# Kernel optimization log

Hardware: AMD Instinct MI355X
Metric: run time of the kernel (lower is better)

Reference implementation:

```python
import jax, jax.numpy as jnp
import numpy as np
from jax import lax

CIN = 3
NUM_BINS = 9
EPS_MAG = 1e-6
EPS_IN = 1e-5  # torch InstanceNorm2d default eps


def setup_inputs() -> dict:
    key = jax.random.key(0)
    kx, = jax.random.split(key, 1)
    x = jax.random.normal(kx, (32, CIN, 512, 512), dtype=jnp.float32)
    # Sobel kernels, repeated across input channels exactly as in _init_weights
    sx = jnp.array([[-1.0, 0.0, 1.0], [-2.0, 0.0, 2.0], [-1.0, 0.0, 1.0]], jnp.float32)
    sy = jnp.array([[-1.0, -2.0, -1.0], [0.0, 0.0, 0.0], [1.0, 2.0, 1.0]], jnp.float32)
    sobel_x = jnp.broadcast_to(sx, (1, CIN, 3, 3)).astype(jnp.float32)  # OIHW
    sobel_y = jnp.broadcast_to(sy, (1, CIN, 3, 3)).astype(jnp.float32)
    # Orientation 1x1 conv weights: [num_bins, 2] = [cos(theta), sin(theta)]
    angles = jnp.linspace(0.0, np.pi, NUM_BINS + 1)[:-1]
    orient_w = jnp.stack([jnp.cos(angles), jnp.sin(angles)], axis=1).astype(jnp.float32)
    # InstanceNorm affine params (torch init: weight=1, bias=0)
    gamma = jnp.ones((NUM_BINS,), jnp.float32)
    beta = jnp.zeros((NUM_BINS,), jnp.float32)
    return {"x": x, "sobel_x": sobel_x, "sobel_y": sobel_y,
            "orient_w": orient_w, "gamma": gamma, "beta": beta}


def _conv3x3(x, w):
    # x: [B,C,H,W], w: [1,C,3,3] -> [B,1,H,W] (padding=1 == SAME)
    return lax.conv_general_dilated(
        x, w, window_strides=(1, 1), padding="SAME",
        dimension_numbers=("NCHW", "OIHW", "NCHW"))


def reference(x, sobel_x, sobel_y, orient_w, gamma, beta):
    # Gradient operator
    gx = _conv3x3(x, sobel_x)  # [B,1,H,W]
    gy = _conv3x3(x, sobel_y)  # [B,1,H,W]
    # Orientation binning
    mag = jnp.sqrt(gx * gx + gy * gy + EPS_MAG)  # [B,1,H,W]
    # 1x1 conv over channels [gx, gy] with weight [K,2] == wx*gx + wy*gy
    wx = orient_w[:, 0][None, :, None, None]
    wy = orient_w[:, 1][None, :, None, None]
    resp = gx * wx + gy * wy  # [B,K,H,W]
    weights = jax.nn.softmax(resp, axis=1)
    binned = mag * weights  # [B,K,H,W]
    # InstanceNorm2d(affine=True): per-(b,c) stats over HxW, biased variance
    mean = jnp.mean(binned, axis=(2, 3), keepdims=True)
    var = jnp.var(binned, axis=(2, 3), keepdims=True)
    xhat = (binned - mean) * lax.rsqrt(var + EPS_IN)
    return xhat * gamma[None, :, None, None] + beta[None, :, None, None]
```

## Files before the change

kernel.cpp:

```cpp
#include <hip/hip_runtime.h>
#include <cstdint>
#include <cstddef>

typedef float f4 __attribute__((ext_vector_type(4)));

constexpr int Bn  = 32;
constexpr int Hh  = 512;
constexpr int Ww  = 512;
constexpr int Kb  = 9;
constexpr float EPS_MAG_F = 1e-6f;
constexpr float EPS_IN_F  = 1e-5f;
constexpr float LOG2E_F   = 1.4426950408889634f;

constexpr int TW = 512;
constexpr int TH = 8;
constexpr int LDS_W = TW + 8;
constexpr int LDS_H = TH + 2;
constexpr int CHUNKS = Hh / TH;
constexpr int BLOCKS_PER_IMG = CHUNKS;
constexpr int NSLOT = LDS_H * (LDS_W / 4);

#if __has_builtin(__builtin_amdgcn_exp2f)
#define EXP2F(x) __builtin_amdgcn_exp2f(x)
#else
#define EXP2F(x) exp2f(x)
#endif
#if __has_builtin(__builtin_amdgcn_sqrtf)
#define SQRTF(x) __builtin_amdgcn_sqrtf(x)
#else
#define SQRTF(x) sqrtf(x)
#endif
#if __has_builtin(__builtin_amdgcn_rcpf)
#define RCPF(x) __builtin_amdgcn_rcpf(x)
#else
#define RCPF(x) (1.0f / (x))
#endif

struct RowW { float hd[4]; float hs[4]; };

template <int PASS>
__global__ __launch_bounds__(256) void goe_tile_kernel(
    const float* __restrict__ x,
    const float* __restrict__ s_in,
    float* __restrict__ s_out,
    const float* __restrict__ orient_w,
    const float2* __restrict__ stats,
    float* __restrict__ partial,
    float* __restrict__ out)
{
    __shared__ float sm[LDS_H][LDS_W];

    const int b  = blockIdx.y;
    const int h0 = blockIdx.x * TH;
    const int tx = threadIdx.x;
    const int ty = threadIdx.y;
    const int tid = ty * 128 + tx;
    const int lane = tid & 63;

    const size_t plane = (size_t)Hh * Ww;
    const float* xb = x + (size_t)b * 3 * plane;

#pragma unroll
    for (int it = 0; it < 6; ++it) {
        const int slot = tid + it * 256;
        if (slot < NSLOT) {
            const int row = slot / 130;
            const int q   = slot - row * 130;
            const int gh  = h0 - 1 + row;
            const int gw  = q * 4 - 4;
            const bool ok = (unsigned)gh < (unsigned)Hh && (unsigned)gw < (unsigned)Ww;
            f4 v = {0.f, 0.f, 0.f, 0.f};
            if (PASS == 0) {
                if (ok) {
                    const float* p = xb + (size_t)gh * Ww + gw;
                    const f4 a = *(const f4*)(p);
                    const f4 c = *(const f4*)(p + plane);
                    const f4 d = *(const f4*)(p + 2 * plane);
                    v = a + c + d;
                }
                *(f4*)&sm[row][q * 4] = v;
                if ((unsigned)(row - 1) < (unsigned)TH && (unsigned)(q - 1) < 128u) {
                    *(f4*)&s_out[((size_t)b * Hh + gh) * Ww + gw] = v;
                }
            } else {
                if (ok) v = *(const f4*)&s_in[((size_t)b * Hh + gh) * Ww + gw];
                *(f4*)&sm[row][q * 4] = v;
            }
        }
    }

    float wx2[Kb], wy2[Kb];
#pragma unroll
    for (int k = 0; k < Kb; ++k) {
        wx2[k] = orient_w[2 * k]     * LOG2E_F;
        wy2[k] = orient_w[2 * k + 1] * LOG2E_F;
    }

    float2 st[Kb];
    if (PASS == 1) {
#pragma unroll
        for (int k = 0; k < Kb; ++k) st[k] = stats[b * Kb + k];
    }

    float accs[Kb], accq[Kb];
    if (PASS == 0) {
#pragma unroll
        for (int k = 0; k < Kb; ++k) { accs[k] = 0.f; accq[k] = 0.f; }
    }

    __syncthreads();

    const int cb    = tx * 4;
    const int rbase = ty * 4;

    auto load_row = [&](int sr) -> RowW {
        const f4 m = *(const f4*)&sm[sr][cb + 4];
        float L  = __shfl_up(m.w, 1);
        float Rr = __shfl_down(m.x, 1);
        if (lane == 0)  L  = sm[sr][cb + 3];
        if (lane == 63) Rr = sm[sr][cb + 8];
        RowW r;
        r.hd[0] = m.y - L;   r.hd[1] = m.z - m.x;
        r.hd[2] = m.w - m.y; r.hd[3] = Rr - m.z;
        r.hs[0] = fmaf(2.f, m.x, L + m.y);
        r.hs[1] = fmaf(2.f, m.y, m.x + m.z);
        r.hs[2] = fmaf(2.f, m.z, m.y + m.w);
        r.hs[3] = fmaf(2.f, m.w, m.z + Rr);
        return r;
    };

    auto do_row = [&](const RowW& T, const RowW& M, const RowW& Bo, int rr) {
        float ov[Kb][4];
#pragma unroll
        for (int j = 0; j < 4; ++j) {
            const float gx = fmaf(2.f, M.hd[j], T.hd[j] + Bo.hd[j]);
            const float gy = Bo.hs[j] - T.hs[j];
            const float m2   = fmaf(gx, gx, fmaf(gy, gy, EPS_MAG_F));
            const float mag  = SQRTF(m2);
            const float mag2 = mag * LOG2E_F;
            float e[Kb], se = 0.f;
#pragma unroll
            for (int k = 0; k < Kb; ++k) {
                e[k] = EXP2F(fmaf(gx, wx2[k], fmaf(gy, wy2[k], -mag2)));
                se += e[k];
            }
            const float minv = mag * RCPF(se);
#pragma unroll
            for (int k = 0; k < Kb; ++k) {
                const float bv = e[k] * minv;
                if (PASS == 0) {
                    accs[k] += bv;
                    accq[k] = fmaf(bv, bv, accq[k]);
                } else {
                    ov[k][j] = fmaf(bv, st[k].x, st[k].y);
                }
            }
        }
        if (PASS == 1) {
            const size_t ob = ((size_t)(b * Kb) * Hh + (h0 + rbase + rr)) * Ww + cb;
#pragma unroll
            for (int k = 0; k < Kb; ++k) {
                f4 v4 = {ov[k][0], ov[k][1], ov[k][2], ov[k][3]};
                __builtin_nontemporal_store(v4, (f4*)&out[ob + (size_t)k * plane]);
            }
        }
    };

    RowW A  = load_row(rbase);
    RowW Bf = load_row(rbase + 1);
    RowW Cf = load_row(rbase + 2); do_row(A,  Bf, Cf, 0);
    A  = load_row(rbase + 3);      do_row(Bf, Cf, A,  1);
    Bf = load_row(rbase + 4);      do_row(Cf, A,  Bf, 2);
    Cf = load_row(rbase + 5);      do_row(A,  Bf, Cf, 3);

    if (PASS == 0) {
#pragma unroll
        for (int k = 0; k < Kb; ++k) {
            for (int off = 32; off > 0; off >>= 1) {
                accs[k] += __shfl_down(accs[k], off);
                accq[k] += __shfl_down(accq[k], off);
            }
        }
        __syncthreads();
        float* red = &sm[0][0];
        const int wid = tid >> 6, ln = tid & 63;
        if (ln == 0) {
#pragma unroll
            for (int k = 0; k < Kb; ++k) {
                red[wid * 18 + k]     = accs[k];
                red[wid * 18 + 9 + k] = accq[k];
            }
        }
        __syncthreads();
        if (tid < 18) {
            const float v = red[tid] + red[18 + tid] + red[36 + tid] + red[54 + tid];
            partial[((size_t)b * BLOCKS_PER_IMG + blockIdx.x) * 18 + tid] = v;
        }
    }
}

__global__ __launch_bounds__(64) void goe_stats_kernel(
    const float* __restrict__ partial,
    const float* __restrict__ gamma,
    const float* __restrict__ beta,
    float2* __restrict__ stats)
{
    const int idx = blockIdx.x;
    const int b = idx / Kb, k = idx % Kb;
    const int t = threadIdx.x;

    const float* p = partial + ((size_t)b * BLOCKS_PER_IMG + t) * 18;
    float s = p[k];
    float q = p[9 + k];
    for (int off = 32; off > 0; off >>= 1) {
        s += __shfl_down(s, off);
        q += __shfl_down(q, off);
    }
    if (t == 0) {
        const float invN = 1.f / (float)(Hh * Ww);
        const float mean = s * invN;
        const float var  = fmaxf(q * invN - mean * mean, 0.f);
        const float rstd = rsqrtf(var + EPS_IN_F);
        const float sc   = rstd * gamma[k];
        stats[idx] = make_float2(sc, beta[k] - mean * sc);
    }
}

extern "C" void kernel_launch(void* const* d_in, const int* in_sizes, int n_in,
                              void* d_out, int out_size, void* d_ws, size_t ws_size,
                              hipStream_t stream)
{
    const float* x        = (const float*)d_in[0];
    const float* orient_w = (const float*)d_in[3];
    const float* gamma    = (const float*)d_in[4];
    const float* beta     = (const float*)d_in[5];
    float* out = (float*)d_out;

    float*  s_ws    = (float*)d_ws;
    float*  partial = (float*)((char*)d_ws + (size_t)Bn * Hh * Ww * sizeof(float));
    float2* stats   = (float2*)((char*)partial +
                       (size_t)Bn * BLOCKS_PER_IMG * 18 * sizeof(float));

    const dim3 grid(CHUNKS, Bn);
    const dim3 block(128, 2);

    hipLaunchKernelGGL((goe_tile_kernel<0>), grid, block, 0, stream,
                       x, nullptr, s_ws, orient_w, nullptr, partial, nullptr);
    hipLaunchKernelGGL(goe_stats_kernel, dim3(Bn * Kb), dim3(64), 0, stream,
                       partial, gamma, beta, stats);
    hipLaunchKernelGGL((goe_tile_kernel<1>), grid, block, 0, stream,
                       nullptr, s_ws, nullptr, orient_w, stats, nullptr, out);
}
```

Baseline: 108.0 us.

## Fuse stats and normalize passes into one cooperative kernel with grid sync

Replaces the three-launch pipeline (tile pass 0, stats kernel, tile pass 1) with one cooperative kernel. Each block loads its 16-row tile of the channel-summed input into LDS once, accumulates per-bin sums, syncs the whole grid, reduces the per-image statistics itself, then recomputes the softmax bins from LDS and writes normalized output. This removes the intermediate channel-sum buffer write and re-read plus two kernel launches. In exchange, all 1024 blocks must be resident at once, and the grid-wide barrier serializes the phases. If the cooperative launch fails, the old split path runs as a fallback.

```diff
diff --git a/kernel.cpp b/kernel.cpp
--- a/kernel.cpp
+++ b/kernel.cpp
@@ -1,6 +1,9 @@
 #include <hip/hip_runtime.h>
+#include <hip/hip_cooperative_groups.h>
 #include <cstdint>
 #include <cstddef>
+
+namespace cg = cooperative_groups;
 
 typedef float f4 __attribute__((ext_vector_type(4)));
 
@@ -11,14 +14,6 @@
 constexpr float EPS_MAG_F = 1e-6f;
 constexpr float EPS_IN_F  = 1e-5f;
 constexpr float LOG2E_F   = 1.4426950408889634f;
-
-constexpr int TW = 512;
-constexpr int TH = 8;
-constexpr int LDS_W = TW + 8;
-constexpr int LDS_H = TH + 2;
-constexpr int CHUNKS = Hh / TH;
-constexpr int BLOCKS_PER_IMG = CHUNKS;
-constexpr int NSLOT = LDS_H * (LDS_W / 4);
 
 #if __has_builtin(__builtin_amdgcn_exp2f)
 #define EXP2F(x) __builtin_amdgcn_exp2f(x)
@@ -38,8 +33,219 @@
 
 struct RowW { float hd[4]; float hs[4]; };
 
+constexpr int FTH     = 16;
+constexpr int FCHUNKS = Hh / FTH;
+constexpr int FLDS_H  = FTH + 2;
+
+__global__ __launch_bounds__(256, 4) void goe_fused_kernel(
+    const float* __restrict__ x,
+    const float* __restrict__ orient_w,
+    const float* __restrict__ gamma,
+    const float* __restrict__ beta,
+    float* __restrict__ partial,
+    float* __restrict__ out)
+{
+    __shared__ float sm[FLDS_H][Ww];
+    __shared__ float red2[FCHUNKS * 18];
+    __shared__ float sums[18];
+    __shared__ float2 stsh[Kb];
+
+    const int bx    = blockIdx.x;
+    const int b     = bx >> 5;
+    const int chunk = bx & (FCHUNKS - 1);
+    const int h0    = chunk * FTH;
+    const int tid   = threadIdx.x;
+    const int tx    = tid & 127;
+    const int ty    = tid >> 7;
+    const int lane  = tid & 63;
+
+    const size_t plane = (size_t)Hh * Ww;
+    const float* xb = x + (size_t)b * 3 * plane;
+
+#pragma unroll
+    for (int it = 0; it < 9; ++it) {
+        const int slot = tid + it * 256;
+        const int row  = slot >> 7;
+        const int q    = slot & 127;
+        const int gh   = h0 - 1 + row;
+        f4 v = {0.f, 0.f, 0.f, 0.f};
+        if ((unsigned)gh < (unsigned)Hh) {
+            const float* p = xb + (size_t)gh * Ww + q * 4;
+            v = *(const f4*)(p) + *(const f4*)(p + plane) + *(const f4*)(p + 2 * plane);
+        }
+        *(f4*)&sm[row][q * 4] = v;
+    }
+
+    float wx2[Kb], wy2[Kb];
+#pragma unroll
+    for (int k = 0; k < Kb; ++k) {
+        wx2[k] = orient_w[2 * k]     * LOG2E_F;
+        wy2[k] = orient_w[2 * k + 1] * LOG2E_F;
+    }
+
+    __syncthreads();
+
+    const int cb = tx * 4;
+    const int s0 = ty * 8;
+
+    auto load_row = [&](int sr) -> RowW {
+        const f4 m = *(const f4*)&sm[sr][cb];
+        float L  = __shfl_up(m.w, 1);
+        float Rr = __shfl_down(m.x, 1);
+        if (lane == 0)  L  = (tx == 0)   ? 0.f : sm[sr][cb - 1];
+        if (lane == 63) Rr = (tx == 127) ? 0.f : sm[sr][cb + 4];
+        RowW r;
+        r.hd[0] = m.y - L;   r.hd[1] = m.z - m.x;
+        r.hd[2] = m.w - m.y; r.hd[3] = Rr - m.z;
+        r.hs[0] = fmaf(2.f, m.x, L + m.y);
+        r.hs[1] = fmaf(2.f, m.y, m.x + m.z);
+        r.hs[2] = fmaf(2.f, m.z, m.y + m.w);
+        r.hs[3] = fmaf(2.f, m.w, m.z + Rr);
+        return r;
+    };
+
+    float accs[Kb], accq[Kb];
+#pragma unroll
+    for (int k = 0; k < Kb; ++k) { accs[k] = 0.f; accq[k] = 0.f; }
+
+    auto acc_row = [&](const RowW& T, const RowW& M, const RowW& Bo) {
+#pragma unroll
+        for (int j = 0; j < 4; ++j) {
+            const float gx = fmaf(2.f, M.hd[j], T.hd[j] + Bo.hd[j]);
+            const float gy = Bo.hs[j] - T.hs[j];
+            const float m2   = fmaf(gx, gx, fmaf(gy, gy, EPS_MAG_F));
+            const float mag  = SQRTF(m2);
+            const float mag2 = mag * LOG2E_F;
+            float e[Kb], se = 0.f;
+#pragma unroll
+            for (int k = 0; k < Kb; ++k) {
+                e[k] = EXP2F(fmaf(gx, wx2[k], fmaf(gy, wy2[k], -mag2)));
+                se += e[k];
+            }
+            const float minv = mag * RCPF(se);
+#pragma unroll
+            for (int k = 0; k < Kb; ++k) {
+                const float bv = e[k] * minv;
+                accs[k] += bv;
+                accq[k] = fmaf(bv, bv, accq[k]);
+            }
+        }
+    };
+
+    {
+        RowW A  = load_row(s0);
+        RowW Bf = load_row(s0 + 1);
+        RowW Cf = load_row(s0 + 2); acc_row(A,  Bf, Cf);
+        A  = load_row(s0 + 3);      acc_row(Bf, Cf, A);
+        Bf = load_row(s0 + 4);      acc_row(Cf, A,  Bf);
+        Cf = load_row(s0 + 5);      acc_row(A,  Bf, Cf);
+        A  = load_row(s0 + 6);      acc_row(Bf, Cf, A);
+        Bf = load_row(s0 + 7);      acc_row(Cf, A,  Bf);
+        Cf = load_row(s0 + 8);      acc_row(A,  Bf, Cf);
+        A  = load_row(s0 + 9);      acc_row(Bf, Cf, A);
+    }
+
+#pragma unroll
+    for (int k = 0; k < Kb; ++k) {
+        for (int off = 32; off > 0; off >>= 1) {
+            accs[k] += __shfl_down(accs[k], off);
+            accq[k] += __shfl_down(accq[k], off);
+        }
+    }
+    const int wid = tid >> 6;
+    if (lane == 0) {
+#pragma unroll
+        for (int k = 0; k < Kb; ++k) {
+            red2[wid * 18 + k]     = accs[k];
+            red2[wid * 18 + 9 + k] = accq[k];
+        }
+    }
+    __syncthreads();
+    if (tid < 18) {
+        const float v = red2[tid] + red2[18 + tid] + red2[36 + tid] + red2[54 + tid];
+        partial[((size_t)b * FCHUNKS + chunk) * 18 + tid] = v;
+    }
+    __threadfence();
+
+    cg::this_grid().sync();
+    __threadfence();
+
+    for (int idx = tid; idx < FCHUNKS * 18; idx += 256)
+        red2[idx] = partial[(size_t)b * (FCHUNKS * 18) + idx];
+    __syncthreads();
+    if (tid < 18) {
+        float s = 0.f;
+#pragma unroll
+        for (int blk = 0; blk < FCHUNKS; ++blk) s += red2[blk * 18 + tid];
+        sums[tid] = s;
+    }
+    __syncthreads();
+    if (tid < Kb) {
+        const float invN = 1.f / (float)(Hh * Ww);
+        const float mean = sums[tid] * invN;
+        const float var  = fmaxf(sums[9 + tid] * invN - mean * mean, 0.f);
+        const float rstd = rsqrtf(var + EPS_IN_F);
+        const float sc   = rstd * gamma[tid];
+        stsh[tid] = make_float2(sc, beta[tid] - mean * sc);
+    }
+    __syncthreads();
+
+    float2 st[Kb];
+#pragma unroll
+    for (int k = 0; k < Kb; ++k) st[k] = stsh[k];
+
+    auto out_row = [&](const RowW& T, const RowW& M, const RowW& Bo, int rr) {
+        float ov[Kb][4];
+#pragma unroll
+        for (int j = 0; j < 4; ++j) {
+            const float gx = fmaf(2.f, M.hd[j], T.hd[j] + Bo.hd[j]);
+            const float gy = Bo.hs[j] - T.hs[j];
+            const float m2   = fmaf(gx, gx, fmaf(gy, gy, EPS_MAG_F));
+            const float mag  = SQRTF(m2);
+            const float mag2 = mag * LOG2E_F;
+            float e[Kb], se = 0.f;
+#pragma unroll
+            for (int k = 0; k < Kb; ++k) {
+                e[k] = EXP2F(fmaf(gx, wx2[k], fmaf(gy, wy2[k], -mag2)));
+                se += e[k];
+            }
+            const float minv = mag * RCPF(se);
+#pragma unroll
+            for (int k = 0; k < Kb; ++k) {
+                ov[k][j] = fmaf(e[k] * minv, st[k].x, st[k].y);
+            }
+        }
+        const int r_img = h0 + ty * 8 + rr;
+        const size_t ob = ((size_t)(b * Kb) * Hh + r_img) * Ww + cb;
+#pragma unroll
+        for (int k = 0; k < Kb; ++k) {
+            f4 v4 = {ov[k][0], ov[k][1], ov[k][2], ov[k][3]};
+            __builtin_nontemporal_store(v4, (f4*)&out[ob + (size_t)k * plane]);
+        }
+    };
+
+    {
+        RowW A  = load_row(s0);
+        RowW Bf = load_row(s0 + 1);
+        RowW Cf = load_row(s0 + 2); out_row(A,  Bf, Cf, 0);
+        A  = load_row(s0 + 3);      out_row(Bf, Cf, A,  1);
+        Bf = load_row(s0 + 4);      out_row(Cf, A,  Bf, 2);
+        Cf = load_row(s0 + 5);      out_row(A,  Bf, Cf, 3);
+        A  = load_row(s0 + 6);      out_row(Bf, Cf, A,  4);
+        Bf = load_row(s0 + 7);      out_row(Cf, A,  Bf, 5);
+        Cf = load_row(s0 + 8);      out_row(A,  Bf, Cf, 6);
+        A  = load_row(s0 + 9);      out_row(Bf, Cf, A,  7);
+    }
+}
+
+constexpr int STH    = 8;
+constexpr int SLDS_W = Ww + 8;
+constexpr int SLDS_H = STH + 2;
+constexpr int SCHUNKS = Hh / STH;
+constexpr int SNSLOT  = SLDS_H * (SLDS_W / 4);
+
 template <int PASS>
-__global__ __launch_bounds__(256) void goe_tile_kernel(
+__global__ __launch_bounds__(256) void goe_split_kernel(
     const float* __restrict__ x,
     const float* __restrict__ s_in,
     float* __restrict__ s_out,
@@ -48,10 +254,10 @@
     float* __restrict__ partial,
     float* __restrict__ out)
 {
-    __shared__ float sm[LDS_H][LDS_W];
+    __shared__ float sm[SLDS_H][SLDS_W];
 
     const int b  = blockIdx.y;
-    const int h0 = blockIdx.x * TH;
+    const int h0 = blockIdx.x * STH;
     const int tx = threadIdx.x;
     const int ty = threadIdx.y;
     const int tid = ty * 128 + tx;
@@ -63,7 +269,7 @@
 #pragma unroll
     for (int it = 0; it < 6; ++it) {
         const int slot = tid + it * 256;
-        if (slot < NSLOT) {
+        if (slot < SNSLOT) {
             const int row = slot / 130;
             const int q   = slot - row * 130;
             const int gh  = h0 - 1 + row;
@@ -73,13 +279,10 @@
             if (PASS == 0) {
                 if (ok) {
                     const float* p = xb + (size_t)gh * Ww + gw;
-                    const f4 a = *(const f4*)(p);
-                    const f4 c = *(const f4*)(p + plane);
-                    const f4 d = *(const f4*)(p + 2 * plane);
-                    v = a + c + d;
+                    v = *(const f4*)(p) + *(const f4*)(p + plane) + *(const f4*)(p + 2 * plane);
                 }
                 *(f4*)&sm[row][q * 4] = v;
-                if ((unsigned)(row - 1) < (unsigned)TH && (unsigned)(q - 1) < 128u) {
+                if ((unsigned)(row - 1) < (unsigned)STH && (unsigned)(q - 1) < 128u) {
                     *(f4*)&s_out[((size_t)b * Hh + gh) * Ww + gw] = v;
                 }
             } else {
@@ -194,7 +397,7 @@
         __syncthreads();
         if (tid < 18) {
             const float v = red[tid] + red[18 + tid] + red[36 + tid] + red[54 + tid];
-            partial[((size_t)b * BLOCKS_PER_IMG + blockIdx.x) * 18 + tid] = v;
+            partial[((size_t)b * SCHUNKS + blockIdx.x) * 18 + tid] = v;
         }
     }
 }
@@ -209,7 +412,7 @@
     const int b = idx / Kb, k = idx % Kb;
     const int t = threadIdx.x;
 
-    const float* p = partial + ((size_t)b * BLOCKS_PER_IMG + t) * 18;
+    const float* p = partial + ((size_t)b * SCHUNKS + t) * 18;
     float s = p[k];
     float q = p[9 + k];
     for (int off = 32; off > 0; off >>= 1) {
@@ -234,20 +437,30 @@
     const float* orient_w = (const float*)d_in[3];
     const float* gamma    = (const float*)d_in[4];
     const float* beta     = (const float*)d_in[5];
-    float* out = (float*)d_out;
+    float* outp = (float*)d_out;
+
+    float* fpartial = (float*)d_ws;
+
+    void* args[] = {(void*)&x, (void*)&orient_w, (void*)&gamma, (void*)&beta,
+                    (void*)&fpartial, (void*)&outp};
+    hipError_t err = hipLaunchCooperativeKernel((void*)goe_fused_kernel,
+                                                dim3(Bn * FCHUNKS), dim3(256),
+                                                args, 0, stream);
+    if (err == hipSuccess) return;
+    (void)hipGetLastError();
 
     float*  s_ws    = (float*)d_ws;
     float*  partial = (float*)((char*)d_ws + (size_t)Bn * Hh * Ww * sizeof(float));
     float2* stats   = (float2*)((char*)partial +
-                       (size_t)Bn * BLOCKS_PER_IMG * 18 * sizeof(float));
-
-    const dim3 grid(CHUNKS, Bn);
+                       (size_t)Bn * SCHUNKS * 18 * sizeof(float));
+
+    const dim3 grid(SCHUNKS, Bn);
     const dim3 block(128, 2);
 
-    hipLaunchKernelGGL((goe_tile_kernel<0>), grid, block, 0, stream,
+    hipLaunchKernelGGL((goe_split_kernel<0>), grid, block, 0, stream,
                        x, nullptr, s_ws, orient_w, nullptr, partial, nullptr);
     hipLaunchKernelGGL(goe_stats_kernel, dim3(Bn * Kb), dim3(64), 0, stream,
                        partial, gamma, beta, stats);
-    hipLaunchKernelGGL((goe_tile_kernel<1>), grid, block, 0, stream,
-                       nullptr, s_ws, nullptr, orient_w, stats, nullptr, out);
+    hipLaunchKernelGGL((goe_split_kernel<1>), grid, block, 0, stream,
+                       nullptr, s_ws, nullptr, orient_w, stats, nullptr, outp);
 }
```

Result: slower. 267.4 us (+147.5%).

## Fold stats reduction into pass0 via last-block atomic counter, drop stats kernel

Applied to the files above, without the earlier changes.

Removes the separate stats kernel. The last pass0 block per image, found with an atomic counter, reduces the partial sums and writes the normalization stats. A memset launch is added to reset the counters. The output stores in pass1 also change from nontemporal to normal stores, which may change cache behaviour on the large output write.

```diff
diff --git a/kernel.cpp b/kernel.cpp
--- a/kernel.cpp
+++ b/kernel.cpp
@@ -12,13 +12,12 @@
 constexpr float EPS_IN_F  = 1e-5f;
 constexpr float LOG2E_F   = 1.4426950408889634f;
 
-constexpr int TW = 512;
-constexpr int TH = 8;
-constexpr int LDS_W = TW + 8;
-constexpr int LDS_H = TH + 2;
-constexpr int CHUNKS = Hh / TH;
-constexpr int BLOCKS_PER_IMG = CHUNKS;
-constexpr int NSLOT = LDS_H * (LDS_W / 4);
+constexpr int STH    = 8;
+constexpr int SLDS_W = Ww + 8;
+constexpr int SLDS_H = STH + 2;
+constexpr int SCHUNKS = Hh / STH;
+constexpr int SNSLOT  = SLDS_H * (SLDS_W / 4);
+constexpr int CNT_STRIDE_U32 = 16;
 
 #if __has_builtin(__builtin_amdgcn_exp2f)
 #define EXP2F(x) __builtin_amdgcn_exp2f(x)
@@ -38,20 +37,21 @@
 
 struct RowW { float hd[4]; float hs[4]; };
 
-template <int PASS>
-__global__ __launch_bounds__(256) void goe_tile_kernel(
+__global__ __launch_bounds__(256) void goe_pass0_kernel(
     const float* __restrict__ x,
-    const float* __restrict__ s_in,
     float* __restrict__ s_out,
     const float* __restrict__ orient_w,
-    const float2* __restrict__ stats,
+    const float* __restrict__ gamma,
+    const float* __restrict__ beta,
+    unsigned int* __restrict__ cnt,
     float* __restrict__ partial,
-    float* __restrict__ out)
+    float2* __restrict__ stats)
 {
-    __shared__ float sm[LDS_H][LDS_W];
+    __shared__ float sm[SLDS_H][SLDS_W];
+    __shared__ int is_last;
 
     const int b  = blockIdx.y;
-    const int h0 = blockIdx.x * TH;
+    const int h0 = blockIdx.x * STH;
     const int tx = threadIdx.x;
     const int ty = threadIdx.y;
     const int tid = ty * 128 + tx;
@@ -63,28 +63,20 @@
 #pragma unroll
     for (int it = 0; it < 6; ++it) {
         const int slot = tid + it * 256;
-        if (slot < NSLOT) {
+        if (slot < SNSLOT) {
             const int row = slot / 130;
             const int q   = slot - row * 130;
             const int gh  = h0 - 1 + row;
             const int gw  = q * 4 - 4;
             const bool ok = (unsigned)gh < (unsigned)Hh && (unsigned)gw < (unsigned)Ww;
             f4 v = {0.f, 0.f, 0.f, 0.f};
-            if (PASS == 0) {
-                if (ok) {
-                    const float* p = xb + (size_t)gh * Ww + gw;
-                    const f4 a = *(const f4*)(p);
-                    const f4 c = *(const f4*)(p + plane);
-                    const f4 d = *(const f4*)(p + 2 * plane);
-                    v = a + c + d;
-                }
-                *(f4*)&sm[row][q * 4] = v;
-                if ((unsigned)(row - 1) < (unsigned)TH && (unsigned)(q - 1) < 128u) {
-                    *(f4*)&s_out[((size_t)b * Hh + gh) * Ww + gw] = v;
-                }
-            } else {
-                if (ok) v = *(const f4*)&s_in[((size_t)b * Hh + gh) * Ww + gw];
-                *(f4*)&sm[row][q * 4] = v;
+            if (ok) {
+                const float* p = xb + (size_t)gh * Ww + gw;
+                v = *(const f4*)(p) + *(const f4*)(p + plane) + *(const f4*)(p + 2 * plane);
+            }
+            *(f4*)&sm[row][q * 4] = v;
+            if ((unsigned)(row - 1) < (unsigned)STH && (unsigned)(q - 1) < 128u) {
+                *(f4*)&s_out[((size_t)b * Hh + gh) * Ww + gw] = v;
             }
         }
     }
@@ -96,17 +88,9 @@
         wy2[k] = orient_w[2 * k + 1] * LOG2E_F;
     }
 
-    float2 st[Kb];
-    if (PASS == 1) {
-#pragma unroll
-        for (int k = 0; k < Kb; ++k) st[k] = stats[b * Kb + k];
-    }
-
     float accs[Kb], accq[Kb];
-    if (PASS == 0) {
-#pragma unroll
-        for (int k = 0; k < Kb; ++k) { accs[k] = 0.f; accq[k] = 0.f; }
-    }
+#pragma unroll
+    for (int k = 0; k < Kb; ++k) { accs[k] = 0.f; accq[k] = 0.f; }
 
     __syncthreads();
 
@@ -129,8 +113,7 @@
         return r;
     };
 
-    auto do_row = [&](const RowW& T, const RowW& M, const RowW& Bo, int rr) {
-        float ov[Kb][4];
+    auto acc_row = [&](const RowW& T, const RowW& M, const RowW& Bo) {
 #pragma unroll
         for (int j = 0; j < 4; ++j) {
             const float gx = fmaf(2.f, M.hd[j], T.hd[j] + Bo.hd[j]);
@@ -148,21 +131,169 @@
 #pragma unroll
             for (int k = 0; k < Kb; ++k) {
                 const float bv = e[k] * minv;
-                if (PASS == 0) {
-                    accs[k] += bv;
-                    accq[k] = fmaf(bv, bv, accq[k]);
-                } else {
-                    ov[k][j] = fmaf(bv, st[k].x, st[k].y);
-                }
-            }
-        }
-        if (PASS == 1) {
-            const size_t ob = ((size_t)(b * Kb) * Hh + (h0 + rbase + rr)) * Ww + cb;
+                accs[k] += bv;
+                accq[k] = fmaf(bv, bv, accq[k]);
+            }
+        }
+    };
+
+    {
+        RowW A  = load_row(rbase);
+        RowW Bf = load_row(rbase + 1);
+        RowW Cf = load_row(rbase + 2); acc_row(A,  Bf, Cf);
+        A  = load_row(rbase + 3);      acc_row(Bf, Cf, A);
+        Bf = load_row(rbase + 4);      acc_row(Cf, A,  Bf);
+        Cf = load_row(rbase + 5);      acc_row(A,  Bf, Cf);
+    }
+
+#pragma unroll
+    for (int k = 0; k < Kb; ++k) {
+        for (int off = 32; off > 0; off >>= 1) {
+            accs[k] += __shfl_down(accs[k], off);
+            accq[k] += __shfl_down(accq[k], off);
+        }
+    }
+    __syncthreads();
+    float* scratch = &sm[0][0];
+    const int wid = tid >> 6;
+    if (lane == 0) {
+#pragma unroll
+        for (int k = 0; k < Kb; ++k) {
+            scratch[wid * 18 + k]     = accs[k];
+            scratch[wid * 18 + 9 + k] = accq[k];
+        }
+    }
+    __syncthreads();
+    if (tid < 18) {
+        const float v = scratch[tid] + scratch[18 + tid] +
+                        scratch[36 + tid] + scratch[54 + tid];
+        __hip_atomic_store(&partial[((size_t)b * SCHUNKS + blockIdx.x) * 18 + tid],
+                           v, __ATOMIC_RELAXED, __HIP_MEMORY_SCOPE_AGENT);
+    }
+    __syncthreads();
+
+    if (tid == 0) {
+        const unsigned old = __hip_atomic_fetch_add(
+            &cnt[b * CNT_STRIDE_U32], 1u,
+            __ATOMIC_ACQ_REL, __HIP_MEMORY_SCOPE_AGENT);
+        is_last = (old == (unsigned)(SCHUNKS - 1));
+    }
+    __syncthreads();
+    if (!is_last) return;
+
+    __builtin_amdgcn_fence(__ATOMIC_ACQUIRE, "agent");
+    for (int idx = tid; idx < SCHUNKS * 18; idx += 256)
+        scratch[idx] = __hip_atomic_load(
+            &partial[(size_t)b * (SCHUNKS * 18) + idx],
+            __ATOMIC_RELAXED, __HIP_MEMORY_SCOPE_AGENT);
+    __syncthreads();
+    if (tid < 18) {
+        float s = 0.f;
+#pragma unroll
+        for (int blk = 0; blk < SCHUNKS; ++blk) s += scratch[blk * 18 + tid];
+        scratch[SCHUNKS * 18 + tid] = s;
+    }
+    __syncthreads();
+    if (tid < Kb) {
+        const float invN = 1.f / (float)(Hh * Ww);
+        const float mean = scratch[SCHUNKS * 18 + tid] * invN;
+        const float var  = fmaxf(scratch[SCHUNKS * 18 + 9 + tid] * invN
+                                 - mean * mean, 0.f);
+        const float rstd = rsqrtf(var + EPS_IN_F);
+        const float sc   = rstd * gamma[tid];
+        stats[b * Kb + tid] = make_float2(sc, beta[tid] - mean * sc);
+    }
+}
+
+__global__ __launch_bounds__(256) void goe_pass1_kernel(
+    const float* __restrict__ s_in,
+    const float* __restrict__ orient_w,
+    const float2* __restrict__ stats,
+    float* __restrict__ out)
+{
+    __shared__ float sm[SLDS_H][SLDS_W];
+
+    const int b  = blockIdx.y;
+    const int h0 = blockIdx.x * STH;
+    const int tx = threadIdx.x;
+    const int ty = threadIdx.y;
+    const int tid = ty * 128 + tx;
+    const int lane = tid & 63;
+
+    const size_t plane = (size_t)Hh * Ww;
+
+#pragma unroll
+    for (int it = 0; it < 6; ++it) {
+        const int slot = tid + it * 256;
+        if (slot < SNSLOT) {
+            const int row = slot / 130;
+            const int q   = slot - row * 130;
+            const int gh  = h0 - 1 + row;
+            const int gw  = q * 4 - 4;
+            const bool ok = (unsigned)gh < (unsigned)Hh && (unsigned)gw < (unsigned)Ww;
+            f4 v = {0.f, 0.f, 0.f, 0.f};
+            if (ok) v = *(const f4*)&s_in[((size_t)b * Hh + gh) * Ww + gw];
+            *(f4*)&sm[row][q * 4] = v;
+        }
+    }
+
+    float wx2[Kb], wy2[Kb];
+#pragma unroll
+    for (int k = 0; k < Kb; ++k) {
+        wx2[k] = orient_w[2 * k]     * LOG2E_F;
+        wy2[k] = orient_w[2 * k + 1] * LOG2E_F;
+    }
+    float2 st[Kb];
+#pragma unroll
+    for (int k = 0; k < Kb; ++k) st[k] = stats[b * Kb + k];
+
+    __syncthreads();
+
+    const int cb    = tx * 4;
+    const int rbase = ty * 4;
+
+    auto load_row = [&](int sr) -> RowW {
+        const f4 m = *(const f4*)&sm[sr][cb + 4];
+        float L  = __shfl_up(m.w, 1);
+        float Rr = __shfl_down(m.x, 1);
+        if (lane == 0)  L  = sm[sr][cb + 3];
+        if (lane == 63) Rr = sm[sr][cb + 8];
+        RowW r;
+        r.hd[0] = m.y - L;   r.hd[1] = m.z - m.x;
+        r.hd[2] = m.w - m.y; r.hd[3] = Rr - m.z;
+        r.hs[0] = fmaf(2.f, m.x, L + m.y);
+        r.hs[1] = fmaf(2.f, m.y, m.x + m.z);
+        r.hs[2] = fmaf(2.f, m.z, m.y + m.w);
+        r.hs[3] = fmaf(2.f, m.w, m.z + Rr);
+        return r;
+    };
+
+    auto do_row = [&](const RowW& T, const RowW& M, const RowW& Bo, int rr) {
+        float ov[Kb][4];
+#pragma unroll
+        for (int j = 0; j < 4; ++j) {
+            const float gx = fmaf(2.f, M.hd[j], T.hd[j] + Bo.hd[j]);
+            const float gy = Bo.hs[j] - T.hs[j];
+            const float m2   = fmaf(gx, gx, fmaf(gy, gy, EPS_MAG_F));
+            const float mag  = SQRTF(m2);
+            const float mag2 = mag * LOG2E_F;
+            float e[Kb], se = 0.f;
 #pragma unroll
             for (int k = 0; k < Kb; ++k) {
-                f4 v4 = {ov[k][0], ov[k][1], ov[k][2], ov[k][3]};
-                __builtin_nontemporal_store(v4, (f4*)&out[ob + (size_t)k * plane]);
-            }
+                e[k] = EXP2F(fmaf(gx, wx2[k], fmaf(gy, wy2[k], -mag2)));
+                se += e[k];
+            }
+            const float minv = mag * RCPF(se);
+#pragma unroll
+            for (int k = 0; k < Kb; ++k) {
+                ov[k][j] = fmaf(e[k] * minv, st[k].x, st[k].y);
+            }
+        }
+        const size_t ob = ((size_t)(b * Kb) * Hh + (h0 + rbase + rr)) * Ww + cb;
+#pragma unroll
+        for (int k = 0; k < Kb; ++k) {
+            f4 v4 = {ov[k][0], ov[k][1], ov[k][2], ov[k][3]};
+            *(f4*)&out[ob + (size_t)k * plane] = v4;
         }
     };
 
@@ -172,58 +303,6 @@
     A  = load_row(rbase + 3);      do_row(Bf, Cf, A,  1);
     Bf = load_row(rbase + 4);      do_row(Cf, A,  Bf, 2);
     Cf = load_row(rbase + 5);      do_row(A,  Bf, Cf, 3);
-
-    if (PASS == 0) {
-#pragma unroll
-        for (int k = 0; k < Kb; ++k) {
-            for (int off = 32; off > 0; off >>= 1) {
-                accs[k] += __shfl_down(accs[k], off);
-                accq[k] += __shfl_down(accq[k], off);
-            }
-        }
-        __syncthreads();
-        float* red = &sm[0][0];
-        const int wid = tid >> 6, ln = tid & 63;
-        if (ln == 0) {
-#pragma unroll
-            for (int k = 0; k < Kb; ++k) {
-                red[wid * 18 + k]     = accs[k];
-                red[wid * 18 + 9 + k] = accq[k];
-            }
-        }
-        __syncthreads();
-        if (tid < 18) {
-            const float v = red[tid] + red[18 + tid] + red[36 + tid] + red[54 + tid];
-            partial[((size_t)b * BLOCKS_PER_IMG + blockIdx.x) * 18 + tid] = v;
-        }
-    }
-}
-
-__global__ __launch_bounds__(64) void goe_stats_kernel(
-    const float* __restrict__ partial,
-    const float* __restrict__ gamma,
-    const float* __restrict__ beta,
-    float2* __restrict__ stats)
-{
-    const int idx = blockIdx.x;
-    const int b = idx / Kb, k = idx % Kb;
-    const int t = threadIdx.x;
-
-    const float* p = partial + ((size_t)b * BLOCKS_PER_IMG + t) * 18;
-    float s = p[k];
-    float q = p[9 + k];
-    for (int off = 32; off > 0; off >>= 1) {
-        s += __shfl_down(s, off);
-        q += __shfl_down(q, off);
-    }
-    if (t == 0) {
-        const float invN = 1.f / (float)(Hh * Ww);
-        const float mean = s * invN;
-        const float var  = fmaxf(q * invN - mean * mean, 0.f);
-        const float rstd = rsqrtf(var + EPS_IN_F);
-        const float sc   = rstd * gamma[k];
-        stats[idx] = make_float2(sc, beta[k] - mean * sc);
-    }
 }
 
 extern "C" void kernel_launch(void* const* d_in, const int* in_sizes, int n_in,
@@ -234,20 +313,21 @@
     const float* orient_w = (const float*)d_in[3];
     const float* gamma    = (const float*)d_in[4];
     const float* beta     = (const float*)d_in[5];
-    float* out = (float*)d_out;
-
-    float*  s_ws    = (float*)d_ws;
-    float*  partial = (float*)((char*)d_ws + (size_t)Bn * Hh * Ww * sizeof(float));
-    float2* stats   = (float2*)((char*)partial +
-                       (size_t)Bn * BLOCKS_PER_IMG * 18 * sizeof(float));
-
-    const dim3 grid(CHUNKS, Bn);
+    float* outp = (float*)d_out;
+
+    unsigned int* cnt = (unsigned int*)d_ws;
+    float*  sidecar   = (float*)((char*)d_ws + 2048);
+    float*  partial   = (float*)((char*)sidecar + (size_t)Bn * Hh * Ww * sizeof(float));
+    float2* stats     = (float2*)((char*)partial +
+                        (size_t)Bn * SCHUNKS * 18 * sizeof(float));
+
+    (void)hipMemsetAsync(d_ws, 0, 2048, stream);
+
+    const dim3 grid(SCHUNKS, Bn);
     const dim3 block(128, 2);
 
-    hipLaunchKernelGGL((goe_tile_kernel<0>), grid, block, 0, stream,
-                       x, nullptr, s_ws, orient_w, nullptr, partial, nullptr);
-    hipLaunchKernelGGL(goe_stats_kernel, dim3(Bn * Kb), dim3(64), 0, stream,
-                       partial, gamma, beta, stats);
-    hipLaunchKernelGGL((goe_tile_kernel<1>), grid, block, 0, stream,
-                       nullptr, s_ws, nullptr, orient_w, stats, nullptr, out);
+    hipLaunchKernelGGL(goe_pass0_kernel, grid, block, 0, stream,
+                       x, sidecar, orient_w, gamma, beta, cnt, partial, stats);
+    hipLaunchKernelGGL(goe_pass1_kernel, grid, block, 0, stream,
+                       sidecar, orient_w, stats, outp);
 }
```

After: 176.8 us. 1.64x slower.
